# Performance work log

Hardware: AMD Instinct MI355X
Metric: run time of the kernel (lower is better)

## Reference

```python
import jax, jax.numpy as jnp
import numpy as np

D_MODEL = 4096
N_EXPERTS = 64
TOP_K = 8
EPS = 1e-9


def setup_inputs() -> dict:
    key = jax.random.key(0)
    kx, kw = jax.random.split(key)
    x = jax.random.normal(kx, (4, 4096, D_MODEL), dtype=jnp.float32)
    # nn.Linear(d_model, n_experts, bias=False): weight shape [n_experts, d_model]
    W = jax.random.normal(kw, (N_EXPERTS, D_MODEL), dtype=jnp.float32) * (1.0 / np.sqrt(D_MODEL))
    return {"x": x, "W": W}


def reference(x, W):
    # flatten [B,S,D] -> [N,D]
    if x.ndim == 3:
        x = x.reshape(-1, x.shape[-1])
    logits = jnp.einsum('nd,ed->ne', x, W)          # [N, E]
    probs = jax.nn.softmax(logits, axis=-1)          # [N, E]
    top_val, top_idx = jax.lax.top_k(probs, TOP_K)   # [N, K] each
    weights = top_val / (jnp.sum(top_val, axis=-1, keepdims=True) + EPS)
    return top_idx, weights, probs
```

## Files before the change

kernel.cpp:

```cpp
#include <hip/hip_runtime.h>
#include <math.h>


constexpr int D  = 4096;
constexpr int E  = 64;
constexpr int K  = 8;
constexpr int BT = 128;
constexpr int BK = 32;
constexpr int CS = 132;

typedef const unsigned int __attribute__((address_space(1))) gu32;
typedef unsigned int       __attribute__((address_space(3))) lu32;

__device__ __forceinline__ void gload16(const float* src, float* lds_dst)
{
    __builtin_amdgcn_global_load_lds((gu32*)src, (lu32*)lds_dst, 16, 0, 0);
}

__global__ __launch_bounds__(128, 2) void router_gemm(
    const float* __restrict__ x, const float* __restrict__ W,
    float* __restrict__ partial, int ntok, int dlen, int ntiles)
{
    __shared__ float smem[8448];

    const int tid   = threadIdx.x;
    const int tile  = blockIdx.x % ntiles;
    const int chunk = blockIdx.x / ntiles;
    const int t0 = tile * BT;
    const int d0 = chunk * dlen;

    const int l   = tid & 63;
    const int wv  = tid >> 6;
    const int lr  = l >> 3;
    const int lc  = l & 7;
    const int swc = lc ^ lr;

    const float* xgw = x + (size_t)(t0 + wv * 64 + lr) * D + d0 + swc * 4;
    const float* wgw = W + (size_t)(wv * 32 + lr) * D + d0 + swc * 4;
    char* xlds = (char*)smem + wv * 8192;
    char* wlds = (char*)smem + 16384 + wv * 4096;

    const int tx  = tid & 7;
    const int ty  = tid >> 3;
    const int ty7 = ty & 7;
    const char* xrd = (const char*)smem + ty * 128;
    const char* wrd = (const char*)smem + 16384 + tx * 128;

    float acc[8][8];
#pragma unroll
    for (int i = 0; i < 8; ++i)
#pragma unroll
        for (int j = 0; j < 8; ++j) acc[i][j] = 0.f;

    const int nk = dlen / BK;
    for (int k = 0; k < nk; ++k) {
        __syncthreads();
        {
            const float* p = xgw + (size_t)k * BK;
#pragma unroll
            for (int ww = 0; ww < 8; ++ww) {
                gload16(p, (float*)(xlds + ww * 1024));
                p += (size_t)8 * D;
            }
            const float* q = wgw + (size_t)k * BK;
#pragma unroll
            for (int ww = 0; ww < 4; ++ww) {
                gload16(q, (float*)(wlds + ww * 1024));
                q += (size_t)8 * D;
            }
        }
        __syncthreads();

#pragma unroll
        for (int d4 = 0; d4 < 8; ++d4) {
            float4 xf[8];
            const int cx = (d4 ^ ty7) * 16;
#pragma unroll
            for (int i = 0; i < 8; ++i)
                xf[i] = *(const float4*)(xrd + i * 2048 + cx);
            const int cw = (d4 ^ tx) * 16;
#pragma unroll
            for (int j = 0; j < 8; ++j) {
                const float4 wf = *(const float4*)(wrd + j * 1024 + cw);
#pragma unroll
                for (int i = 0; i < 8; ++i) {
                    float a = acc[i][j];
                    a = fmaf(xf[i].x, wf.x, a);
                    a = fmaf(xf[i].y, wf.y, a);
                    a = fmaf(xf[i].z, wf.z, a);
                    a = fmaf(xf[i].w, wf.w, a);
                    acc[i][j] = a;
                }
            }
        }
    }

    __syncthreads();
    float* cs = smem;
#pragma unroll
    for (int j = 0; j < 8; ++j)
#pragma unroll
        for (int i = 0; i < 8; ++i)
            cs[(tx + 8 * j) * CS + (ty + 16 * i)] = acc[i][j];
    __syncthreads();

#pragma unroll
    for (int jj = 0; jj < 32; ++jj) {
        const int e = wv * 32 + jj;
        float* dst = partial + ((size_t)chunk * E + e) * ntok + t0;
        dst[l]      = cs[e * CS + l];
        dst[l + 64] = cs[e * CS + l + 64];
    }
}

template <int NC>
__global__ __launch_bounds__(256) void router_finish(
    const float* __restrict__ partial, float* __restrict__ out, int ntok)
{
    __shared__ float ls[64][E + 4];

    const int tid = threadIdx.x;
    const int t0  = blockIdx.x * 64;
    const int t   = tid & 63;
    const int eg  = tid >> 6;

#pragma unroll
    for (int j = 0; j < 16; ++j) {
        const int e = eg * 16 + j;
        const float* p = partial + (size_t)e * ntok + t0 + t;
        float v = p[0];
#pragma unroll
        for (int c = 1; c < NC; ++c)
            v += p[(size_t)c * E * ntok];
        ls[t][e] = v;
    }
    __syncthreads();

    if (tid < 64) {
        const int n = t0 + tid;
        float l[E];
#pragma unroll
        for (int g = 0; g < 16; ++g) {
            const float4 v = *(const float4*)&ls[tid][g * 4];
            l[g * 4 + 0] = v.x; l[g * 4 + 1] = v.y;
            l[g * 4 + 2] = v.z; l[g * 4 + 3] = v.w;
        }

        float m = l[0];
#pragma unroll
        for (int e = 1; e < E; ++e) m = fmaxf(m, l[e]);
        float sum = 0.f;
#pragma unroll
        for (int e = 0; e < E; ++e) { l[e] = expf(l[e] - m); sum += l[e]; }
        const float inv = 1.f / sum;
#pragma unroll
        for (int e = 0; e < E; ++e) l[e] *= inv;

        float* probs = out + (size_t)ntok * 2 * K + (size_t)n * E;
#pragma unroll
        for (int g = 0; g < 16; ++g)
            *(float4*)&probs[g * 4] =
                make_float4(l[g * 4], l[g * 4 + 1], l[g * 4 + 2], l[g * 4 + 3]);

        float vals[K];
        int   idxs[K];
        float ts = 0.f;
        for (int k = 0; k < K; ++k) {
            float best = -1.f;
            int   bi   = 0;
#pragma unroll
            for (int e = 0; e < E; ++e)
                if (l[e] > best) { best = l[e]; bi = e; }
            vals[k] = best;
            idxs[k] = bi;
            ts += best;
#pragma unroll
            for (int e = 0; e < E; ++e)
                if (e == bi) l[e] = -1.f;
        }
        const float winv = 1.f / (ts + 1e-9f);

        float* oi = out + (size_t)n * K;
        float* ow = out + (size_t)ntok * K + (size_t)n * K;
#pragma unroll
        for (int k = 0; k < K; ++k) {
            oi[k] = (float)idxs[k];
            ow[k] = vals[k] * winv;
        }
    }
}

extern "C" void kernel_launch(void* const* d_in, const int* in_sizes, int n_in,
                              void* d_out, int out_size, void* d_ws, size_t ws_size,
                              hipStream_t stream)
{
    const float* x = (const float*)d_in[0];
    const float* W = (const float*)d_in[1];
    float* out = (float*)d_out;

    const int ntok = in_sizes[0] / D;

    int nchunks = 8;
    while (nchunks > 1 &&
           (size_t)nchunks * E * (size_t)ntok * sizeof(float) > ws_size)
        nchunks >>= 1;
    const int dlen   = D / nchunks;
    const int ntiles = ntok / BT;

    float* partial = (float*)d_ws;

    hipLaunchKernelGGL(router_gemm, dim3(ntiles * nchunks), dim3(128), 0, stream,
                       x, W, partial, ntok, dlen, ntiles);
    switch (nchunks) {
        case 8:
            hipLaunchKernelGGL(router_finish<8>, dim3(ntok / 64), dim3(256), 0,
                               stream, partial, out, ntok);
            break;
        case 4:
            hipLaunchKernelGGL(router_finish<4>, dim3(ntok / 64), dim3(256), 0,
                               stream, partial, out, ntok);
            break;
        case 2:
            hipLaunchKernelGGL(router_finish<2>, dim3(ntok / 64), dim3(256), 0,
                               stream, partial, out, ntok);
            break;
        default:
            hipLaunchKernelGGL(router_finish<1>, dim3(ntok / 64), dim3(256), 0,
                               stream, partial, out, ntok);
            break;
    }
}
```

Measured before the change: 412.2 us.

## Double-buffer router GEMM K-loop and parallelize finish softmax/top-k across lanes

The GEMM now uses BK=16 with two LDS buffers and issues the async global-to-LDS load of the next tile before computing the current one. This is meant to hide global memory latency that the single-buffered loop previously exposed. The finish kernel loads partial sums as float4 and spreads each token's 64 logits over 4 lanes, doing softmax and top-k with shuffle reductions instead of using only 64 of 256 threads. Smaller K tiles double the number of barriers per unit of work. The LDS layout and swizzle changed, which could introduce bank conflicts.

```diff
diff --git a/kernel.cpp b/kernel.cpp
--- a/kernel.cpp
+++ b/kernel.cpp
@@ -6,7 +6,7 @@
 constexpr int E  = 64;
 constexpr int K  = 8;
 constexpr int BT = 128;
-constexpr int BK = 32;
+constexpr int BK = 16;
 constexpr int CS = 132;
 
 typedef const unsigned int __attribute__((address_space(1))) gu32;
@@ -31,20 +31,17 @@
 
     const int l   = tid & 63;
     const int wv  = tid >> 6;
-    const int lr  = l >> 3;
-    const int lc  = l & 7;
-    const int swc = lc ^ lr;
-
-    const float* xgw = x + (size_t)(t0 + wv * 64 + lr) * D + d0 + swc * 4;
-    const float* wgw = W + (size_t)(wv * 32 + lr) * D + d0 + swc * 4;
-    char* xlds = (char*)smem + wv * 8192;
-    char* wlds = (char*)smem + 16384 + wv * 4096;
+    const int lr  = l >> 2;
+    const int lc  = l & 3;
+    const int swc = lc ^ (lr & 3);
+
+    const float* xg = x + (size_t)(t0 + wv * 64 + lr) * D + d0 + swc * 4;
+    const float* wg = W + (size_t)(wv * 32 + lr) * D + d0 + swc * 4;
 
     const int tx  = tid & 7;
     const int ty  = tid >> 3;
-    const int ty7 = ty & 7;
-    const char* xrd = (const char*)smem + ty * 128;
-    const char* wrd = (const char*)smem + 16384 + tx * 128;
+    const int tym = (ty & 3);
+    const int txm = (tx & 3);
 
     float acc[8][8];
 #pragma unroll
@@ -53,47 +50,60 @@
         for (int j = 0; j < 8; ++j) acc[i][j] = 0.f;
 
     const int nk = dlen / BK;
-    for (int k = 0; k < nk; ++k) {
+
+#define STAGE(kk, b)                                                         \
+    {                                                                        \
+        const float* px = xg + (size_t)(kk) * BK;                            \
+        float* bx = smem + (b) * 2048 + wv * 1024;                           \
+        gload16(px,                     bx);                                 \
+        gload16(px + (size_t)16 * D,    bx + 256);                           \
+        gload16(px + (size_t)32 * D,    bx + 512);                           \
+        gload16(px + (size_t)48 * D,    bx + 768);                           \
+        const float* pw = wg + (size_t)(kk) * BK;                            \
+        float* bw = smem + 4096 + (b) * 1024 + wv * 512;                     \
+        gload16(pw,                     bw);                                 \
+        gload16(pw + (size_t)16 * D,    bw + 256);                           \
+    }
+
+#define COMPUTE(b)                                                           \
+    {                                                                        \
+        const float* xb = smem + (b) * 2048 + ty * 16;                       \
+        const float* wb = smem + 4096 + (b) * 1024 + tx * 16;                \
+        _Pragma("unroll")                                                    \
+        for (int d4 = 0; d4 < 4; ++d4) {                                     \
+            const int cxo = (d4 ^ tym) * 4;                                  \
+            float4 xf[8];                                                    \
+            _Pragma("unroll")                                                \
+            for (int i = 0; i < 8; ++i)                                      \
+                xf[i] = *(const float4*)(xb + i * 256 + cxo);                \
+            const int cwo = (d4 ^ txm) * 4;                                  \
+            _Pragma("unroll")                                                \
+            for (int j = 0; j < 8; ++j) {                                    \
+                const float4 wf = *(const float4*)(wb + j * 128 + cwo);      \
+                _Pragma("unroll")                                            \
+                for (int i = 0; i < 8; ++i) {                                \
+                    float a = acc[i][j];                                     \
+                    a = fmaf(xf[i].x, wf.x, a);                              \
+                    a = fmaf(xf[i].y, wf.y, a);                              \
+                    a = fmaf(xf[i].z, wf.z, a);                              \
+                    a = fmaf(xf[i].w, wf.w, a);                              \
+                    acc[i][j] = a;                                           \
+                }                                                            \
+            }                                                                \
+        }                                                                    \
+    }
+
+    STAGE(0, 0);
+    for (int k = 0; k + 2 <= nk; k += 2) {
         __syncthreads();
-        {
-            const float* p = xgw + (size_t)k * BK;
-#pragma unroll
-            for (int ww = 0; ww < 8; ++ww) {
-                gload16(p, (float*)(xlds + ww * 1024));
-                p += (size_t)8 * D;
-            }
-            const float* q = wgw + (size_t)k * BK;
-#pragma unroll
-            for (int ww = 0; ww < 4; ++ww) {
-                gload16(q, (float*)(wlds + ww * 1024));
-                q += (size_t)8 * D;
-            }
-        }
+        STAGE(k + 1, 1);
+        COMPUTE(0);
         __syncthreads();
-
-#pragma unroll
-        for (int d4 = 0; d4 < 8; ++d4) {
-            float4 xf[8];
-            const int cx = (d4 ^ ty7) * 16;
-#pragma unroll
-            for (int i = 0; i < 8; ++i)
-                xf[i] = *(const float4*)(xrd + i * 2048 + cx);
-            const int cw = (d4 ^ tx) * 16;
-#pragma unroll
-            for (int j = 0; j < 8; ++j) {
-                const float4 wf = *(const float4*)(wrd + j * 1024 + cw);
-#pragma unroll
-                for (int i = 0; i < 8; ++i) {
-                    float a = acc[i][j];
-                    a = fmaf(xf[i].x, wf.x, a);
-                    a = fmaf(xf[i].y, wf.y, a);
-                    a = fmaf(xf[i].z, wf.z, a);
-                    a = fmaf(xf[i].w, wf.w, a);
-                    acc[i][j] = a;
-                }
-            }
-        }
-    }
+        if (k + 2 < nk) STAGE(k + 2, 0);
+        COMPUTE(1);
+    }
+#undef STAGE
+#undef COMPUTE
 
     __syncthreads();
     float* cs = smem;
@@ -121,65 +131,87 @@
 
     const int tid = threadIdx.x;
     const int t0  = blockIdx.x * 64;
-    const int t   = tid & 63;
-    const int eg  = tid >> 6;
-
-#pragma unroll
-    for (int j = 0; j < 16; ++j) {
-        const int e = eg * 16 + j;
-        const float* p = partial + (size_t)e * ntok + t0 + t;
-        float v = p[0];
-#pragma unroll
-        for (int c = 1; c < NC; ++c)
-            v += p[(size_t)c * E * ntok];
-        ls[t][e] = v;
+
+    const int t4 = tid & 15;
+    const int eb = tid >> 4;
+#pragma unroll
+    for (int g = 0; g < 4; ++g) {
+        const int e = eb + 16 * g;
+        const float* p = partial + (size_t)e * ntok + t0 + t4 * 4;
+        float4 a = *(const float4*)p;
+#pragma unroll
+        for (int c = 1; c < NC; ++c) {
+            const float4 b = *(const float4*)(p + (size_t)c * E * ntok);
+            a.x += b.x; a.y += b.y; a.z += b.z; a.w += b.w;
+        }
+        ls[t4 * 4 + 0][e] = a.x;
+        ls[t4 * 4 + 1][e] = a.y;
+        ls[t4 * 4 + 2][e] = a.z;
+        ls[t4 * 4 + 3][e] = a.w;
     }
     __syncthreads();
 
-    if (tid < 64) {
-        const int n = t0 + tid;
-        float l[E];
-#pragma unroll
-        for (int g = 0; g < 16; ++g) {
-            const float4 v = *(const float4*)&ls[tid][g * 4];
-            l[g * 4 + 0] = v.x; l[g * 4 + 1] = v.y;
-            l[g * 4 + 2] = v.z; l[g * 4 + 3] = v.w;
-        }
-
-        float m = l[0];
-#pragma unroll
-        for (int e = 1; e < E; ++e) m = fmaxf(m, l[e]);
-        float sum = 0.f;
-#pragma unroll
-        for (int e = 0; e < E; ++e) { l[e] = expf(l[e] - m); sum += l[e]; }
-        const float inv = 1.f / sum;
-#pragma unroll
-        for (int e = 0; e < E; ++e) l[e] *= inv;
-
-        float* probs = out + (size_t)ntok * 2 * K + (size_t)n * E;
-#pragma unroll
-        for (int g = 0; g < 16; ++g)
-            *(float4*)&probs[g * 4] =
-                make_float4(l[g * 4], l[g * 4 + 1], l[g * 4 + 2], l[g * 4 + 3]);
-
-        float vals[K];
-        int   idxs[K];
-        float ts = 0.f;
-        for (int k = 0; k < K; ++k) {
-            float best = -1.f;
-            int   bi   = 0;
-#pragma unroll
-            for (int e = 0; e < E; ++e)
-                if (l[e] > best) { best = l[e]; bi = e; }
-            vals[k] = best;
-            idxs[k] = bi;
-            ts += best;
-#pragma unroll
-            for (int e = 0; e < E; ++e)
-                if (e == bi) l[e] = -1.f;
-        }
-        const float winv = 1.f / (ts + 1e-9f);
-
+    const int tt = tid >> 2;
+    const int q  = tid & 3;
+    const int n  = t0 + tt;
+
+    float v[16];
+#pragma unroll
+    for (int g = 0; g < 4; ++g) {
+        const float4 r = *(const float4*)&ls[tt][q * 16 + g * 4];
+        v[g * 4 + 0] = r.x; v[g * 4 + 1] = r.y;
+        v[g * 4 + 2] = r.z; v[g * 4 + 3] = r.w;
+    }
+
+    float m = v[0];
+#pragma unroll
+    for (int e = 1; e < 16; ++e) m = fmaxf(m, v[e]);
+    m = fmaxf(m, __shfl_xor(m, 1));
+    m = fmaxf(m, __shfl_xor(m, 2));
+
+    float s = 0.f;
+#pragma unroll
+    for (int e = 0; e < 16; ++e) { v[e] = expf(v[e] - m); s += v[e]; }
+    s += __shfl_xor(s, 1);
+    s += __shfl_xor(s, 2);
+    const float inv = 1.f / s;
+#pragma unroll
+    for (int e = 0; e < 16; ++e) v[e] *= inv;
+
+    float* probs = out + (size_t)ntok * 2 * K + (size_t)n * E;
+#pragma unroll
+    for (int g = 0; g < 4; ++g)
+        *(float4*)&probs[q * 16 + g * 4] =
+            make_float4(v[g * 4], v[g * 4 + 1], v[g * 4 + 2], v[g * 4 + 3]);
+
+    float vals[K];
+    int   idxs[K];
+    float ts = 0.f;
+    for (int k = 0; k < K; ++k) {
+        float b  = v[0];
+        int   bi = q * 16;
+#pragma unroll
+        for (int e = 1; e < 16; ++e)
+            if (v[e] > b) { b = v[e]; bi = q * 16 + e; }
+        float ob;
+        int   obi;
+        ob  = __shfl_xor(b, 1);
+        obi = __shfl_xor(bi, 1);
+        if (ob > b || (ob == b && obi < bi)) { b = ob; bi = obi; }
+        ob  = __shfl_xor(b, 2);
+        obi = __shfl_xor(bi, 2);
+        if (ob > b || (ob == b && obi < bi)) { b = ob; bi = obi; }
+        vals[k] = b;
+        idxs[k] = bi;
+        ts += b;
+        const int lo = bi - q * 16;
+#pragma unroll
+        for (int e = 0; e < 16; ++e)
+            if (e == lo) v[e] = -1.f;
+    }
+    const float winv = 1.f / (ts + 1e-9f);
+
+    if (q == 0) {
         float* oi = out + (size_t)n * K;
         float* ow = out + (size_t)ntok * K + (size_t)n * K;
 #pragma unroll
```

New measurement: 748.2 us. +81.5%, slower.
